# Kernel optimization log

Measured on AMD Instinct MI355X. Metric: run time of the kernel, lower is better.

Reference implementation:

```python
import jax, jax.numpy as jnp
import numpy as np

HEAD_DIM = 128
SCALE = 1.0 / np.sqrt(HEAD_DIM)  # standard 1/sqrt(d) attention scaling


def setup_inputs() -> dict:
    key = jax.random.key(0)
    kq, kk, kv = jax.random.split(key, 3)
    q = jax.random.normal(kq, (2, 32, 2048, HEAD_DIM), dtype=jnp.float16)
    k = jax.random.normal(kk, (2, 8, 2048, HEAD_DIM), dtype=jnp.float16)
    v = jax.random.normal(kv, (2, 8, 2048, HEAD_DIM), dtype=jnp.float16)
    return {"q": q, "k": k, "v": v}


def reference(q, k, v):
    # GQA attention: each of the g = H // KVH query heads in a group attends
    # against the group's single shared K/V head (no K/V duplication).
    b, h, sq, d = q.shape
    kvh = k.shape[1]
    g = h // kvh
    # [b, kvh, g, sq, d] -- group-packed Q, mirroring the kernel's _pack_q
    qg = q.reshape(b, kvh, g, sq, d)
    # fp32 accumulation as in flash-attention kernels
    scores = jnp.einsum(
        'bhgqd,bhkd->bhgqk',
        qg.astype(jnp.float32), k.astype(jnp.float32)) * SCALE
    p = jax.nn.softmax(scores, axis=-1)  # non-causal, full attention
    o = jnp.einsum('bhgqk,bhkd->bhgqd', p, v.astype(jnp.float32))
    return o.reshape(b, h, sq, d).astype(q.dtype)
```

## Files before the change

kernel.cpp:

```cpp
#include <hip/hip_runtime.h>

#define SEQ   2048
#define HD    128
#define BN    64
#define NITER (SEQ / BN)

typedef __fp16 f16x8  __attribute__((ext_vector_type(8)));
typedef float  f32x4  __attribute__((ext_vector_type(4)));
typedef float  f32x16 __attribute__((ext_vector_type(16)));

__device__ __forceinline__ unsigned pkh(float a, float b) {
  auto h = __builtin_amdgcn_cvt_pkrtz(a, b);
  return __builtin_bit_cast(unsigned, h);
}

__global__ __launch_bounds__(256, 2)
void fa_gqa_kernel(const float* __restrict__ Q,
                   const float* __restrict__ K,
                   const float* __restrict__ V,
                   float* __restrict__ O)
{
  __shared__ unsigned short kt_lds[64 * HD];
  __shared__ unsigned short vt_lds[HD * 64];

  const int tid  = threadIdx.x;
  const int lane = tid & 63;
  const int w    = tid >> 6;
  const int ml   = lane & 31;
  const int hi   = lane >> 5;
  const bool hib = (hi != 0);

  const int F     = blockIdx.x;
  const int xcd   = F & 7;
  const int s     = F >> 3;
  const int bh    = xcd * 8 + (s >> 4);
  const int qtile = s & 15;

  const int b = bh >> 5;
  const int h = bh & 31;
  const long qrow0 = (long)bh * SEQ + qtile * 128 + w * 32;
  const float* Qw = Q + qrow0 * HD;
  float*       Ow = O + qrow0 * HD;
  const long kvoff = (long)(b * 8 + (h >> 2)) * SEQ * HD;
  const float* Kb = K + kvoff;
  const float* Vb = V + kvoff;

  f16x8 qf[8];
#pragma unroll
  for (int dc = 0; dc < 8; ++dc) {
    const float4* qp = (const float4*)(Qw + ml * HD + dc * 16 + hi * 8);
    float4 a = qp[0], bq = qp[1];
    int4 t;
    t.x = (int)pkh(a.x, a.y);
    t.y = (int)pkh(a.z, a.w);
    t.z = (int)pkh(bq.x, bq.y);
    t.w = (int)pkh(bq.z, bq.w);
    qf[dc] = __builtin_bit_cast(f16x8, t);
  }

  f32x16 oacc[4];
#pragma unroll
  for (int dt = 0; dt < 4; ++dt)
    oacc[dt] = (f32x16)(0.f);

  float mst = -1e30f;
  float lst = 0.f;

  const float K1 = 0.08838834764831845f * 1.4426950408889634f;

  const int krow = tid >> 2;
  const int kq4  = tid & 3;
  const int kq   = tid >> 4;
  const int dc8  = tid & 15;

  for (int it = 0; it < NITER; ++it) {
    const int k0 = it * BN;

    const float* kp = Kb + (long)(k0 + krow) * HD + kq4 * 32;
    int4 ks[4];
#pragma unroll
    for (int jj = 0; jj < 4; ++jj) {
      float4 e = ((const float4*)kp)[2 * jj];
      float4 o = ((const float4*)kp)[2 * jj + 1];
      ks[jj].x = (int)pkh(e.x, e.y);
      ks[jj].y = (int)pkh(e.z, e.w);
      ks[jj].z = (int)pkh(o.x, o.y);
      ks[jj].w = (int)pkh(o.z, o.w);
    }

    const float* vp = Vb + (long)(k0 + 4 * kq) * HD + dc8 * 8;
    float4 vr[4][2];
#pragma unroll
    for (int r = 0; r < 4; ++r) {
      vr[r][0] = ((const float4*)(vp + r * HD))[0];
      vr[r][1] = ((const float4*)(vp + r * HD))[1];
    }
    uint2 vs[8];
#pragma unroll
    for (int jd = 0; jd < 8; ++jd) {
      const int hsel = jd >> 2, e = jd & 3;
      float x0 = ((const float*)&vr[0][hsel])[e];
      float x1 = ((const float*)&vr[1][hsel])[e];
      float x2 = ((const float*)&vr[2][hsel])[e];
      float x3 = ((const float*)&vr[3][hsel])[e];
      vs[jd].x = pkh(x0, x1);
      vs[jd].y = pkh(x2, x3);
    }

    __syncthreads();

#pragma unroll
    for (int jj = 0; jj < 4; ++jj) {
      int j = kq4 * 4 + jj;
      int pos = j ^ (krow & 15);
      *(int4*)(kt_lds + krow * HD + pos * 8) = ks[jj];
    }
#pragma unroll
    for (int jd = 0; jd < 8; ++jd) {
      int d = dc8 * 8 + jd;
      int sw3 = ((d >> 3) ^ d) & 7;
      int pos = (kq >> 1) ^ sw3;
      *(uint2*)(vt_lds + d * 64 + pos * 8 + (kq & 1) * 4) = vs[jd];
    }

    __syncthreads();

    f32x16 sacc[2];
    sacc[0] = (f32x16)(0.f);
    sacc[1] = (f32x16)(0.f);

#pragma unroll
    for (int dc = 0; dc < 8; ++dc) {
#pragma unroll
      for (int kt = 0; kt < 2; ++kt) {
        int row = kt * 32 + ml;
        int pos = (2 * dc + hi) ^ (row & 15);
        f16x8 af = *(const f16x8*)(kt_lds + row * HD + pos * 8);
        sacc[kt] = __builtin_amdgcn_mfma_f32_32x32x16_f16(
            af, qf[dc], sacc[kt], 0, 0, 0);
      }
    }

    float mx = sacc[0][0];
#pragma unroll
    for (int kt = 0; kt < 2; ++kt)
#pragma unroll
      for (int r = 0; r < 16; ++r)
        mx = fmaxf(mx, sacc[kt][r]);
    mx = fmaxf(mx, __shfl_xor(mx, 32, 64));
    float mnew = fmaxf(mst, mx);
    float alpha = __builtin_amdgcn_exp2f(K1 * (mst - mnew));
    mst = mnew;
    float nm = -K1 * mnew;
    float sum = 0.f;
#pragma unroll
    for (int kt = 0; kt < 2; ++kt)
#pragma unroll
      for (int r = 0; r < 16; ++r) {
        float p = __builtin_amdgcn_exp2f(fmaf(sacc[kt][r], K1, nm));
        sacc[kt][r] = p;
        sum += p;
      }
    lst = lst * alpha + sum;

#pragma unroll
    for (int dt = 0; dt < 4; ++dt)
      oacc[dt] *= alpha;

#pragma unroll
    for (int st = 0; st < 4; ++st) {
      const int kt = st >> 1;
      const int R  = 8 * (st & 1);
      unsigned pA0 = pkh(sacc[kt][R + 0], sacc[kt][R + 1]);
      unsigned pA1 = pkh(sacc[kt][R + 2], sacc[kt][R + 3]);
      unsigned pB0 = pkh(sacc[kt][R + 4], sacc[kt][R + 5]);
      unsigned pB1 = pkh(sacc[kt][R + 6], sacc[kt][R + 7]);
      unsigned s0 = hib ? pA0 : pB0;
      unsigned s1 = hib ? pA1 : pB1;
      unsigned r0 = (unsigned)__shfl_xor((int)s0, 32, 64);
      unsigned r1 = (unsigned)__shfl_xor((int)s1, 32, 64);
      int4 bf;
      bf.x = (int)(hib ? r0 : pA0);
      bf.y = (int)(hib ? r1 : pA1);
      bf.z = (int)(hib ? pB0 : r0);
      bf.w = (int)(hib ? pB1 : r1);
      f16x8 pfrag = __builtin_bit_cast(f16x8, bf);
#pragma unroll
      for (int dt = 0; dt < 4; ++dt) {
        int d = dt * 32 + ml;
        int pos = (2 * st + hi) ^ (((d >> 3) ^ d) & 7);
        f16x8 vf = *(const f16x8*)(vt_lds + d * 64 + pos * 8);
        oacc[dt] = __builtin_amdgcn_mfma_f32_32x32x16_f16(
            vf, pfrag, oacc[dt], 0, 0, 0);
      }
    }
  }

  float lf = lst + __shfl_xor(lst, 32, 64);
  float linv = 1.0f / lf;
#pragma unroll
  for (int dt = 0; dt < 4; ++dt) {
#pragma unroll
    for (int t = 0; t < 4; ++t) {
      f32x4 ov;
      ov[0] = oacc[dt][4 * t + 0] * linv;
      ov[1] = oacc[dt][4 * t + 1] * linv;
      ov[2] = oacc[dt][4 * t + 2] * linv;
      ov[3] = oacc[dt][4 * t + 3] * linv;
      *(f32x4*)(Ow + ml * HD + dt * 32 + 8 * t + 4 * hi) = ov;
    }
  }
}

extern "C" void kernel_launch(void* const* d_in, const int* in_sizes, int n_in,
                              void* d_out, int out_size, void* d_ws, size_t ws_size,
                              hipStream_t stream) {
  const float* q = (const float*)d_in[0];
  const float* k = (const float*)d_in[1];
  const float* v = (const float*)d_in[2];
  float* o = (float*)d_out;
  fa_gqa_kernel<<<dim3(1024), dim3(256), 0, stream>>>(q, k, v, o);
}
```

Before: 320.2 us.

## Raise occupancy, prioritize MFMA waves, and skip rescale when row max is unchanged

Raises the launch-bounds waves-per-EU hint from 2 to 4, which forces the compiler into a tighter register budget so more blocks can be resident. It brackets both MFMA loops with s_setprio so waves issuing matrix ops get scheduling priority over waves doing softmax. The online-softmax rescale of the output accumulator is skipped when no lane's running max increased, and the max and sum reductions are split into four independent chains to shorten dependency latency. The tighter register cap risks spilling the large f32x16 accumulators, and the new wave-uniform branch adds divergence checks.

```diff
diff --git a/kernel.cpp b/kernel.cpp
--- a/kernel.cpp
+++ b/kernel.cpp
@@ -14,7 +14,7 @@
   return __builtin_bit_cast(unsigned, h);
 }
 
-__global__ __launch_bounds__(256, 2)
+__global__ __launch_bounds__(256, 4)
 void fa_gqa_kernel(const float* __restrict__ Q,
                    const float* __restrict__ K,
                    const float* __restrict__ V,
@@ -129,6 +129,7 @@
     sacc[0] = (f32x16)(0.f);
     sacc[1] = (f32x16)(0.f);
 
+    __builtin_amdgcn_s_setprio(1);
 #pragma unroll
     for (int dc = 0; dc < 8; ++dc) {
 #pragma unroll
@@ -140,32 +141,49 @@
             af, qf[dc], sacc[kt], 0, 0, 0);
       }
     }
-
-    float mx = sacc[0][0];
-#pragma unroll
-    for (int kt = 0; kt < 2; ++kt)
-#pragma unroll
-      for (int r = 0; r < 16; ++r)
-        mx = fmaxf(mx, sacc[kt][r]);
+    __builtin_amdgcn_s_setprio(0);
+
+    float x0 = fmaxf(sacc[0][0], sacc[1][0]);
+    float x1 = fmaxf(sacc[0][1], sacc[1][1]);
+    float x2 = fmaxf(sacc[0][2], sacc[1][2]);
+    float x3 = fmaxf(sacc[0][3], sacc[1][3]);
+#pragma unroll
+    for (int r = 4; r < 16; r += 4) {
+      x0 = fmaxf(x0, fmaxf(sacc[0][r + 0], sacc[1][r + 0]));
+      x1 = fmaxf(x1, fmaxf(sacc[0][r + 1], sacc[1][r + 1]));
+      x2 = fmaxf(x2, fmaxf(sacc[0][r + 2], sacc[1][r + 2]));
+      x3 = fmaxf(x3, fmaxf(sacc[0][r + 3], sacc[1][r + 3]));
+    }
+    float mx = fmaxf(fmaxf(x0, x1), fmaxf(x2, x3));
     mx = fmaxf(mx, __shfl_xor(mx, 32, 64));
-    float mnew = fmaxf(mst, mx);
-    float alpha = __builtin_amdgcn_exp2f(K1 * (mst - mnew));
-    mst = mnew;
-    float nm = -K1 * mnew;
-    float sum = 0.f;
-#pragma unroll
-    for (int kt = 0; kt < 2; ++kt)
-#pragma unroll
-      for (int r = 0; r < 16; ++r) {
-        float p = __builtin_amdgcn_exp2f(fmaf(sacc[kt][r], K1, nm));
-        sacc[kt][r] = p;
-        sum += p;
+
+    if (__any(mx > mst)) {
+      float mnew = fmaxf(mst, mx);
+      float alpha = __builtin_amdgcn_exp2f(K1 * (mst - mnew));
+      mst = mnew;
+      lst *= alpha;
+#pragma unroll
+      for (int dt = 0; dt < 4; ++dt)
+        oacc[dt] *= alpha;
+    }
+
+    const float nm = -K1 * mst;
+    float p0 = 0.f, p1 = 0.f, p2 = 0.f, p3 = 0.f;
+#pragma unroll
+    for (int kt = 0; kt < 2; ++kt) {
+#pragma unroll
+      for (int r = 0; r < 16; r += 4) {
+        float e0 = __builtin_amdgcn_exp2f(fmaf(sacc[kt][r + 0], K1, nm));
+        float e1 = __builtin_amdgcn_exp2f(fmaf(sacc[kt][r + 1], K1, nm));
+        float e2 = __builtin_amdgcn_exp2f(fmaf(sacc[kt][r + 2], K1, nm));
+        float e3 = __builtin_amdgcn_exp2f(fmaf(sacc[kt][r + 3], K1, nm));
+        sacc[kt][r + 0] = e0; p0 += e0;
+        sacc[kt][r + 1] = e1; p1 += e1;
+        sacc[kt][r + 2] = e2; p2 += e2;
+        sacc[kt][r + 3] = e3; p3 += e3;
       }
-    lst = lst * alpha + sum;
-
-#pragma unroll
-    for (int dt = 0; dt < 4; ++dt)
-      oacc[dt] *= alpha;
+    }
+    lst += (p0 + p1) + (p2 + p3);
 
 #pragma unroll
     for (int st = 0; st < 4; ++st) {
@@ -185,6 +203,7 @@
       bf.z = (int)(hib ? pB0 : r0);
       bf.w = (int)(hib ? pB1 : r1);
       f16x8 pfrag = __builtin_bit_cast(f16x8, bf);
+      __builtin_amdgcn_s_setprio(1);
 #pragma unroll
       for (int dt = 0; dt < 4; ++dt) {
         int d = dt * 32 + ml;
@@ -193,6 +212,7 @@
         oacc[dt] = __builtin_amdgcn_mfma_f32_32x32x16_f16(
             vf, pfrag, oacc[dt], 0, 0, 0);
       }
+      __builtin_amdgcn_s_setprio(0);
     }
   }
 
```

Measured after the change: 1.117 ms. +248.9%, slower.
